# Performance work log

Hardware: AMD Instinct MI355X
Metric: run time of the kernel (lower is better)

## Reference

```python
import jax, jax.numpy as jnp
import numpy as np

B, T, TC, C, CC, H = 2, 2048, 512, 1024, 512, 16
D = C // H  # head dim = 64


def setup_inputs() -> dict:
    key = jax.random.key(0)
    ks = jax.random.split(key, 18)
    w = lambda k, i, o: (jax.random.normal(k, (i, o), jnp.float32) / np.sqrt(i).astype(np.float32))
    return {
        "x": jax.random.normal(ks[0], (B, T, C), jnp.float32),
        "cross_input": jax.random.normal(ks[1], (B, TC, CC), jnp.float32),
        "Wk": w(ks[2], C, C),  "bk": jnp.zeros((C,), jnp.float32),
        "Wq": w(ks[3], C, C),  "bq": jnp.zeros((C,), jnp.float32),
        "Wv": w(ks[4], C, C),  "bv": jnp.zeros((C,), jnp.float32),
        "Wck": w(ks[5], CC, C), "bck": jnp.zeros((C,), jnp.float32),
        "Wcq": w(ks[6], C, C),  "bcq": jnp.zeros((C,), jnp.float32),
        "Wcv": w(ks[7], CC, C), "bcv": jnp.zeros((C,), jnp.float32),
        "Wp": w(ks[8], C, C),   "bp": jnp.zeros((C,), jnp.float32),
    }


def _heads(t):
    # [B, L, C] -> [B, H, L, D]
    b, l, _ = t.shape
    return t.reshape(b, l, H, D).transpose(0, 2, 1, 3)


def reference(x, cross_input, Wk, bk, Wq, bq, Wv, bv, Wck, bck, Wcq, bcq, Wcv, bcv, Wp, bp):
    scale = np.float32(1.0 / np.sqrt(D))
    q = _heads(x @ Wq + bq)
    k = _heads(x @ Wk + bk)
    v = _heads(x @ Wv + bv)
    # causal self-attention with materialized scores (faithful to original)
    att = jnp.einsum("bhqd,bhkd->bhqk", q, k) * scale
    causal = jnp.tril(jnp.ones((T, T), bool))
    att = jnp.where(causal[None, None], att, -jnp.inf)
    y = jnp.einsum("bhqk,bhkd->bhqd", jax.nn.softmax(att, axis=-1), v)
    # cross-attention (no mask)
    qc = _heads(x @ Wcq + bcq)
    kc = _heads(cross_input @ Wck + bck)
    vc = _heads(cross_input @ Wcv + bcv)
    attc = jnp.einsum("bhqd,bhkd->bhqk", qc, kc) * scale
    y = y + jnp.einsum("bhqk,bhkd->bhqd", jax.nn.softmax(attc, axis=-1), vc)
    # merge heads + output projection (dropout prob = 0 -> identity)
    y = y.transpose(0, 2, 1, 3).reshape(x.shape[0], T, C)
    return y @ Wp + bp
```

## Files before the change

### kernel.cpp

```cpp
#include <hip/hip_runtime.h>
#include <hip/hip_bf16.h>
#include <type_traits>

typedef __bf16 bf16;
typedef __bf16 bf16x8 __attribute__((ext_vector_type(8)));
typedef float floatx4 __attribute__((ext_vector_type(4)));
typedef unsigned int uint32x4 __attribute__((ext_vector_type(4)));

#if __has_builtin(__builtin_amdgcn_exp2f)
#define EXP2(x) __builtin_amdgcn_exp2f(x)
#else
#define EXP2(x) exp2f(x)
#endif

__device__ __forceinline__ void glds16(const bf16* g, bf16* l) {
  __builtin_amdgcn_global_load_lds((const __attribute__((address_space(1))) void*)g,
                                   (__attribute__((address_space(3))) void*)l, 16, 0, 0);
}

__device__ __forceinline__ unsigned pack_bf16(float a, float b) {
  unsigned short ua = __builtin_bit_cast(unsigned short, (bf16)a);
  unsigned short ub = __builtin_bit_cast(unsigned short, (bf16)b);
  return (unsigned)ua | ((unsigned)ub << 16);
}

struct PrepArgs {
  const float* x; const float* xc;
  bf16* xbf; bf16* xcbf;
  const float* b4[4];
  const float* bc[2];
  float* bias4; float* biasc;
  const float* W[7];
  bf16* WT[7];
};

__global__ __launch_bounds__(256) void prep_kernel(PrepArgs a) {
  __shared__ bf16 tsh[32][33];
  const int bx = blockIdx.x, tid = threadIdx.x;
  if (bx < 4096) {
    int i = bx * 256 + tid;
    float4 f = ((const float4*)a.x)[i];
    bf16 t[4] = {(bf16)f.x, (bf16)f.y, (bf16)f.z, (bf16)f.w};
    *(uint2*)&a.xbf[(long)i * 4] = *(const uint2*)t;
  } else if (bx < 4608) {
    int i = (bx - 4096) * 256 + tid;
    float4 f = ((const float4*)a.xc)[i];
    bf16 t[4] = {(bf16)f.x, (bf16)f.y, (bf16)f.z, (bf16)f.w};
    *(uint2*)&a.xcbf[(long)i * 4] = *(const uint2*)t;
  } else if (bx < 4632) {
    int lb = bx - 4608;
    if (lb < 16) {
      int i = lb * 256 + tid;
      int sec = i >> 10;
      float v = a.b4[sec][i & 1023];
      if (sec == 0 || sec == 3) v *= 0.18033688f;
      a.bias4[i] = v;
    } else {
      int i = (lb - 16) * 256 + tid;
      a.biasc[i] = a.bc[i >> 10][i & 1023];
    }
  } else {
    int t = bx - 4632, w, R, bxw, byw;
    if (t < 5120) { w = t >> 10; R = 1024; int l = t & 1023; bxw = l & 31; byw = l >> 5; }
    else { int t2 = t - 5120; w = 5 + (t2 >> 9); R = 512; int l = t2 & 511; bxw = l & 31; byw = l >> 5; }
    const float* in = a.W[w];
    bf16* out = a.WT[w];
    const float sc = (w == 0 || w == 3) ? 0.18033688f : 1.0f;
    int tx = tid & 31, ty = tid >> 5;
    int c = bxw * 32 + tx;
#pragma unroll
    for (int i = 0; i < 4; i++) {
      int r = byw * 32 + ty + i * 8;
      tsh[ty + i * 8][tx] = (bf16)(in[(long)r * 1024 + c] * sc);
    }
    __syncthreads();
    int oc = byw * 32 + tx;
#pragma unroll
    for (int i = 0; i < 4; i++) {
      int orr = bxw * 32 + ty + i * 8;
      out[(long)orr * R + oc] = tsh[tx][ty + i * 8];
    }
  }
}

template <typename OutT>
__global__ __launch_bounds__(256, 3) void gemm128(const bf16* __restrict__ A,
                                                  const bf16* __restrict__ Bt,
                                                  const float* __restrict__ bias,
                                                  OutT* __restrict__ C,
                                                  int M, int N, int K, int ldc,
                                                  bf16* __restrict__ Vt,
                                                  int vcol0, int vcol1, int Lt, int tok_shift) {
  __shared__ alignas(16) bf16 As[128 * 32];
  __shared__ alignas(16) bf16 Bs[128 * 32];
  const int tid = threadIdx.x, wave = tid >> 6, lane = tid & 63;
  const int l16 = lane & 15, l4 = lane >> 4;
  const int wm = wave & 1, wn = wave >> 1;
  const int n0 = blockIdx.x * 128, m0 = blockIdx.y * 128;
  const int lrow = lane >> 2, lch = (lane & 3) * 8;

  floatx4 acc[4][4];
#pragma unroll
  for (int mt = 0; mt < 4; mt++)
#pragma unroll
    for (int nt = 0; nt < 4; nt++) acc[mt][nt] = (floatx4){0.f, 0.f, 0.f, 0.f};

  const bf16* Ag = A + (long)(m0 + wave * 32 + lrow) * K + lch;
  const bf16* Bg = Bt + (long)(n0 + wave * 32 + lrow) * K + lch;
  bf16* Al = &As[(wave * 32) * 32];
  bf16* Bl = &Bs[(wave * 32) * 32];

  for (int k0 = 0; k0 < K; k0 += 32) {
    __syncthreads();
    glds16(Ag + k0, Al);
    glds16(Ag + k0 + (long)16 * K, Al + 16 * 32);
    glds16(Bg + k0, Bl);
    glds16(Bg + k0 + (long)16 * K, Bl + 16 * 32);
    __syncthreads();
    bf16x8 a[4], b[4];
#pragma unroll
    for (int mt = 0; mt < 4; mt++) a[mt] = *(const bf16x8*)&As[(wm * 64 + mt * 16 + l16) * 32 + l4 * 8];
#pragma unroll
    for (int nt = 0; nt < 4; nt++) b[nt] = *(const bf16x8*)&Bs[(wn * 64 + nt * 16 + l16) * 32 + l4 * 8];
#pragma unroll
    for (int mt = 0; mt < 4; mt++)
#pragma unroll
      for (int nt = 0; nt < 4; nt++)
        acc[mt][nt] = __builtin_amdgcn_mfma_f32_16x16x32_bf16(a[mt], b[nt], acc[mt][nt], 0, 0, 0);
  }

  const bool vpath = (vcol0 >= 0) && (n0 >= vcol0) && (n0 < vcol1);
  if (!vpath) {
    const int coladj = (vcol0 >= 0 && n0 >= vcol1) ? (vcol1 - vcol0) : 0;
#pragma unroll
    for (int nt = 0; nt < 4; nt++) {
      int col = n0 + wn * 64 + nt * 16 + l16;
      float bv = bias[col];
#pragma unroll
      for (int mt = 0; mt < 4; mt++)
#pragma unroll
        for (int r = 0; r < 4; r++) {
          int row = m0 + wm * 64 + mt * 16 + l4 * 4 + r;
          float v = acc[mt][nt][r] + bv;
          if constexpr (std::is_same_v<OutT, float>) C[(long)row * ldc + col - coladj] = v;
          else                                       C[(long)row * ldc + col - coladj] = (bf16)v;
        }
    }
  } else {
#pragma unroll
    for (int nt = 0; nt < 4; nt++) {
      int col = n0 + wn * 64 + nt * 16 + l16;
      int c = col - vcol0, hh = c >> 6, dd = c & 63;
      float bv = bias[col];
#pragma unroll
      for (int mt = 0; mt < 4; mt++) {
        int t0 = m0 + wm * 64 + mt * 16 + l4 * 4;
        int bb = t0 >> tok_shift, t = t0 & ((1 << tok_shift) - 1);
        t = (t & ~31) | (((t >> 2) & 3) << 3) | (((t >> 4) & 1) << 2) | (t & 3);
        bf16 tmp[4];
#pragma unroll
        for (int r = 0; r < 4; r++) tmp[r] = (bf16)(acc[mt][nt][r] + bv);
        *(uint2*)&Vt[(((long)bb * 16 + hh) * 64 + dd) * Lt + t] = *(const uint2*)tmp;
      }
    }
  }
}

__global__ __launch_bounds__(256, 2) void attn_kernel(const bf16* __restrict__ QKQc,
                                                      const bf16* __restrict__ VtB,
                                                      const bf16* __restrict__ KcB,
                                                      const bf16* __restrict__ VctB,
                                                      bf16* __restrict__ Y) {
  __shared__ float2 Mbuf[4][4][16];
  __shared__ alignas(16) bf16 U[4 * 64 * 72];
  const int tid = threadIdx.x, w = tid >> 6, lane = tid & 63;
  const int l16 = lane & 15, l4 = lane >> 4;
  const int bh = blockIdx.x, h = bh & 15, b = bh >> 4;
  const int qt = 31 - (int)blockIdx.y;
  const int q0 = qt * 64;
  const int wk = w * 32;
  const float NEG = -1e30f;

  float o_self[16];

  for (int phase = 0; phase < 2; phase++) {
    const bf16 *Qb, *Kb, *Vtb;
    int kstr, vtstr, nkt;
    if (phase == 0) {
      Qb = QKQc + (long)b * 2048 * 3072 + h * 64;
      Kb = Qb + 1024;                              kstr = 3072;
      Vtb = VtB + ((long)b * 16 + h) * 64 * 2048;  vtstr = 2048;
      nkt = (qt + 2) >> 1;
    } else {
      Qb = QKQc + (long)b * 2048 * 3072 + h * 64 + 2048;
      Kb = KcB + (long)b * 512 * 1024 + h * 64;    kstr = 1024;
      Vtb = VctB + ((long)b * 16 + h) * 64 * 512;  vtstr = 512;
      nkt = 4;
    }

    __syncthreads();

    bf16x8 qf[4][2];
#pragma unroll
    for (int qtt = 0; qtt < 4; qtt++) {
      const bf16* qp = Qb + (long)(q0 + qtt * 16 + l16) * 3072 + l4 * 8;
#pragma unroll
      for (int ds = 0; ds < 2; ds++) qf[qtt][ds] = *(const bf16x8*)(qp + ds * 32);
    }

    float m_i[4], l_i[4];
#pragma unroll
    for (int qtt = 0; qtt < 4; qtt++) { m_i[qtt] = NEG; l_i[qtt] = 0.f; }
    floatx4 oacc[4][4];
#pragma unroll
    for (int mtd = 0; mtd < 4; mtd++)
#pragma unroll
      for (int qtt = 0; qtt < 4; qtt++) oacc[mtd][qtt] = (floatx4){0.f, 0.f, 0.f, 0.f};

    bf16x8 kc[2][2], kn[2][2];
#pragma unroll
    for (int mt = 0; mt < 2; mt++)
#pragma unroll
      for (int ds = 0; ds < 2; ds++)
        kc[mt][ds] = *(const bf16x8*)(Kb + (long)(wk + mt * 16 + l16) * kstr + ds * 32 + l4 * 8);

    for (int kt = 0; kt < nkt; kt++) {
      const int kbase = kt * 128 + wk;
      bf16x8 vc[4];
#pragma unroll
      for (int mtd = 0; mtd < 4; mtd++)
        vc[mtd] = *(const bf16x8*)(Vtb + (long)(mtd * 16 + l16) * vtstr + kbase + l4 * 8);

      floatx4 sacc[2][4];
#pragma unroll
      for (int mt = 0; mt < 2; mt++)
#pragma unroll
        for (int qtt = 0; qtt < 4; qtt++) sacc[mt][qtt] = (floatx4){0.f, 0.f, 0.f, 0.f};
#pragma unroll
      for (int ds = 0; ds < 2; ds++)
#pragma unroll
        for (int mt = 0; mt < 2; mt++)
#pragma unroll
          for (int qtt = 0; qtt < 4; qtt++)
            sacc[mt][qtt] = __builtin_amdgcn_mfma_f32_16x16x32_bf16(kc[mt][ds], qf[qtt][ds], sacc[mt][qtt], 0, 0, 0);

      if (kt + 1 < nkt) {
        const int nb = kbase + 128;
#pragma unroll
        for (int mt = 0; mt < 2; mt++)
#pragma unroll
          for (int ds = 0; ds < 2; ds++)
            kn[mt][ds] = *(const bf16x8*)(Kb + (long)(nb + mt * 16 + l16) * kstr + ds * 32 + l4 * 8);
      }

      if (phase == 0 && kt == nkt - 1) {
#pragma unroll
        for (int mt = 0; mt < 2; mt++) {
          int keyb = kbase + mt * 16 + l4 * 4;
#pragma unroll
          for (int qtt = 0; qtt < 4; qtt++) {
            int q = q0 + qtt * 16 + l16;
#pragma unroll
            for (int r = 0; r < 4; r++)
              if (keyb + r > q) sacc[mt][qtt][r] = NEG;
          }
        }
      }

#pragma unroll
      for (int qtt = 0; qtt < 4; qtt++) {
        float mx = fmaxf(fmaxf(fmaxf(sacc[0][qtt][0], sacc[0][qtt][1]), fmaxf(sacc[0][qtt][2], sacc[0][qtt][3])),
                         fmaxf(fmaxf(sacc[1][qtt][0], sacc[1][qtt][1]), fmaxf(sacc[1][qtt][2], sacc[1][qtt][3])));
        mx = fmaxf(mx, __shfl_xor(mx, 16));
        mx = fmaxf(mx, __shfl_xor(mx, 32));
        float mold = m_i[qtt];
        float nm = fmaxf(mx, mold);
        bool upd = nm > mold + 8.f;
        float al = upd ? EXP2(mold - nm) : 1.f;
        float mcur = upd ? nm : mold;
        m_i[qtt] = mcur;
        float p0 = EXP2(sacc[0][qtt][0] - mcur), p1 = EXP2(sacc[0][qtt][1] - mcur);
        float p2 = EXP2(sacc[0][qtt][2] - mcur), p3 = EXP2(sacc[0][qtt][3] - mcur);
        float p4 = EXP2(sacc[1][qtt][0] - mcur), p5 = EXP2(sacc[1][qtt][1] - mcur);
        float p6 = EXP2(sacc[1][qtt][2] - mcur), p7 = EXP2(sacc[1][qtt][3] - mcur);
        float rs = ((p0 + p1) + (p2 + p3)) + ((p4 + p5) + (p6 + p7));
        rs += __shfl_xor(rs, 16);
        rs += __shfl_xor(rs, 32);
        l_i[qtt] = l_i[qtt] * al + rs;
        if (__any((int)upd)) {
#pragma unroll
          for (int mtd = 0; mtd < 4; mtd++)
#pragma unroll
            for (int r = 0; r < 4; r++) oacc[mtd][qtt][r] *= al;
        }
        uint32x4 pu = {pack_bf16(p0, p1), pack_bf16(p2, p3), pack_bf16(p4, p5), pack_bf16(p6, p7)};
        bf16x8 pf = __builtin_bit_cast(bf16x8, pu);
#pragma unroll
        for (int mtd = 0; mtd < 4; mtd++)
          oacc[mtd][qtt] = __builtin_amdgcn_mfma_f32_16x16x32_bf16(vc[mtd], pf, oacc[mtd][qtt], 0, 0, 0);
      }

#pragma unroll
      for (int mt = 0; mt < 2; mt++)
#pragma unroll
        for (int ds = 0; ds < 2; ds++) kc[mt][ds] = kn[mt][ds];
    }

    if (l4 == 0) {
#pragma unroll
      for (int qtt = 0; qtt < 4; qtt++) Mbuf[w][qtt][l16] = make_float2(m_i[qtt], l_i[qtt]);
    }
    __syncthreads();
    float myscale[4], denom[4];
#pragma unroll
    for (int qtt = 0; qtt < 4; qtt++) {
      float2 s0 = Mbuf[0][qtt][l16], s1 = Mbuf[1][qtt][l16];
      float2 s2 = Mbuf[2][qtt][l16], s3 = Mbuf[3][qtt][l16];
      float M = fmaxf(fmaxf(s0.x, s1.x), fmaxf(s2.x, s3.x));
      denom[qtt] = EXP2(s0.x - M) * s0.y + EXP2(s1.x - M) * s1.y +
                   EXP2(s2.x - M) * s2.y + EXP2(s3.x - M) * s3.y;
      myscale[qtt] = EXP2(m_i[qtt] - M);
    }
#pragma unroll
    for (int qtt = 0; qtt < 4; qtt++)
#pragma unroll
      for (int mtd = 0; mtd < 4; mtd++) {
        float s = myscale[qtt];
        uint2 u = {pack_bf16(oacc[mtd][qtt][0] * s, oacc[mtd][qtt][1] * s),
                   pack_bf16(oacc[mtd][qtt][2] * s, oacc[mtd][qtt][3] * s)};
        *(uint2*)&U[((w * 64) + qtt * 16 + l16) * 72 + mtd * 16 + l4 * 4] = u;
      }
    __syncthreads();
    float sum[16];
#pragma unroll
    for (int j = 0; j < 16; j++) sum[j] = 0.f;
#pragma unroll
    for (int s = 0; s < 4; s++) {
      bf16x8 c0 = *(const bf16x8*)&U[((s * 64) + w * 16 + l16) * 72 + l4 * 16];
      bf16x8 c1 = *(const bf16x8*)&U[((s * 64) + w * 16 + l16) * 72 + l4 * 16 + 8];
#pragma unroll
      for (int j = 0; j < 8; j++) { sum[j] += (float)c0[j]; sum[8 + j] += (float)c1[j]; }
    }
    float invd = 1.0f / denom[w];
    if (phase == 0) {
#pragma unroll
      for (int j = 0; j < 16; j++) o_self[j] = sum[j] * invd;
    } else {
      long row = (long)b * 2048 + q0 + w * 16 + l16;
      bf16 out[16];
#pragma unroll
      for (int j = 0; j < 16; j++) out[j] = (bf16)(o_self[j] + sum[j] * invd);
      *(bf16x8*)&Y[row * 1024 + h * 64 + l4 * 16] = *(const bf16x8*)&out[0];
      *(bf16x8*)&Y[row * 1024 + h * 64 + l4 * 16 + 8] = *(const bf16x8*)&out[8];
    }
  }
}

extern "C" void kernel_launch(void* const* d_in, const int* in_sizes, int n_in,
                              void* d_out, int out_size, void* d_ws, size_t ws_size,
                              hipStream_t stream) {
  const float* x   = (const float*)d_in[0];
  const float* xc  = (const float*)d_in[1];
  const float* Wk  = (const float*)d_in[2];  const float* bk  = (const float*)d_in[3];
  const float* Wq  = (const float*)d_in[4];  const float* bq  = (const float*)d_in[5];
  const float* Wv  = (const float*)d_in[6];  const float* bv  = (const float*)d_in[7];
  const float* Wck = (const float*)d_in[8];  const float* bck = (const float*)d_in[9];
  const float* Wcq = (const float*)d_in[10]; const float* bcq = (const float*)d_in[11];
  const float* Wcv = (const float*)d_in[12]; const float* bcv = (const float*)d_in[13];
  const float* Wp  = (const float*)d_in[14]; const float* bp  = (const float*)d_in[15];

  char* ws = (char*)d_ws;
  const size_t MB = 1ull << 20;
  bf16*  WT_all = (bf16*)(ws + 0);
  bf16*  WC_all = (bf16*)(ws + 8 * MB);
  bf16*  WpT    = (bf16*)(ws + 10 * MB);
  bf16*  xbf    = (bf16*)(ws + 12 * MB);
  bf16*  Yb     = xbf;
  bf16*  xcbf   = (bf16*)(ws + 20 * MB);
  float* bias4  = (float*)(ws + 21 * MB);
  float* biasc  = (float*)(ws + 21 * MB + 65536);
  bf16*  QKQc   = (bf16*)(ws + 22 * MB);
  bf16*  VtB    = (bf16*)(ws + 46 * MB);
  bf16*  KcB    = (bf16*)(ws + 54 * MB);
  bf16*  VctB   = (bf16*)(ws + 56 * MB);

  PrepArgs pa;
  pa.x = x; pa.xc = xc; pa.xbf = xbf; pa.xcbf = xcbf;
  pa.b4[0] = bq; pa.b4[1] = bk; pa.b4[2] = bv; pa.b4[3] = bcq;
  pa.bc[0] = bck; pa.bc[1] = bcv;
  pa.bias4 = bias4; pa.biasc = biasc;
  pa.W[0] = Wq;  pa.WT[0] = WT_all + 0ll * 1024 * 1024;
  pa.W[1] = Wk;  pa.WT[1] = WT_all + 1ll * 1024 * 1024;
  pa.W[2] = Wv;  pa.WT[2] = WT_all + 2ll * 1024 * 1024;
  pa.W[3] = Wcq; pa.WT[3] = WT_all + 3ll * 1024 * 1024;
  pa.W[4] = Wp;  pa.WT[4] = WpT;
  pa.W[5] = Wck; pa.WT[5] = WC_all + 0ll * 1024 * 512;
  pa.W[6] = Wcv; pa.WT[6] = WC_all + 1ll * 1024 * 512;
  prep_kernel<<<10776, 256, 0, stream>>>(pa);

  gemm128<bf16><<<dim3(32, 32), 256, 0, stream>>>(xbf, WT_all, bias4, QKQc,
                                                  4096, 4096, 1024, 3072,
                                                  VtB, 2048, 3072, 2048, 11);
  gemm128<bf16><<<dim3(16, 8), 256, 0, stream>>>(xcbf, WC_all, biasc, KcB,
                                                 1024, 2048, 512, 1024,
                                                 VctB, 1024, 2048, 512, 9);

  attn_kernel<<<dim3(32, 32), 256, 0, stream>>>(QKQc, VtB, KcB, VctB, Yb);

  gemm128<float><<<dim3(8, 32), 256, 0, stream>>>(Yb, WpT, bp, (float*)d_out,
                                                  4096, 1024, 1024, 1024,
                                                  nullptr, -1, -1, 0, 0);
}
```

Measured before the change: 261.7 us.

## Software-pipeline QK^T of next tile with PV MFMAs in attention loop

Restructures the attention inner loop so the QK^T score MFMAs for the next key tile are issued after the softmax of the current tile, alongside the PV MFMAs. The first tile's scores are computed before the loop. This lets the matrix cores overlap with the exp/softmax VALU work, and the double-buffered K registers are reduced to one set. It also raises wave priority around the MFMA burst with s_setprio. The cost is more live registers (sacc and pf held across phases), which could lower occupancy.

```diff
diff --git a/kernel.cpp b/kernel.cpp
--- a/kernel.cpp
+++ b/kernel.cpp
@@ -217,40 +217,42 @@
 #pragma unroll
       for (int qtt = 0; qtt < 4; qtt++) oacc[mtd][qtt] = (floatx4){0.f, 0.f, 0.f, 0.f};
 
-    bf16x8 kc[2][2], kn[2][2];
+    bf16x8 kreg[2][2];
 #pragma unroll
     for (int mt = 0; mt < 2; mt++)
 #pragma unroll
       for (int ds = 0; ds < 2; ds++)
-        kc[mt][ds] = *(const bf16x8*)(Kb + (long)(wk + mt * 16 + l16) * kstr + ds * 32 + l4 * 8);
+        kreg[mt][ds] = *(const bf16x8*)(Kb + (long)(wk + mt * 16 + l16) * kstr + ds * 32 + l4 * 8);
+
+    floatx4 sacc[2][4];
+#pragma unroll
+    for (int mt = 0; mt < 2; mt++)
+#pragma unroll
+      for (int qtt = 0; qtt < 4; qtt++) sacc[mt][qtt] = (floatx4){0.f, 0.f, 0.f, 0.f};
+#pragma unroll
+    for (int ds = 0; ds < 2; ds++)
+#pragma unroll
+      for (int mt = 0; mt < 2; mt++)
+#pragma unroll
+        for (int qtt = 0; qtt < 4; qtt++)
+          sacc[mt][qtt] = __builtin_amdgcn_mfma_f32_16x16x32_bf16(kreg[mt][ds], qf[qtt][ds], sacc[mt][qtt], 0, 0, 0);
 
     for (int kt = 0; kt < nkt; kt++) {
       const int kbase = kt * 128 + wk;
+      const bool more = (kt + 1 < nkt);
+
       bf16x8 vc[4];
 #pragma unroll
       for (int mtd = 0; mtd < 4; mtd++)
         vc[mtd] = *(const bf16x8*)(Vtb + (long)(mtd * 16 + l16) * vtstr + kbase + l4 * 8);
 
-      floatx4 sacc[2][4];
-#pragma unroll
-      for (int mt = 0; mt < 2; mt++)
-#pragma unroll
-        for (int qtt = 0; qtt < 4; qtt++) sacc[mt][qtt] = (floatx4){0.f, 0.f, 0.f, 0.f};
-#pragma unroll
-      for (int ds = 0; ds < 2; ds++)
+      if (more) {
+        const int nb = kbase + 128;
 #pragma unroll
         for (int mt = 0; mt < 2; mt++)
 #pragma unroll
-          for (int qtt = 0; qtt < 4; qtt++)
-            sacc[mt][qtt] = __builtin_amdgcn_mfma_f32_16x16x32_bf16(kc[mt][ds], qf[qtt][ds], sacc[mt][qtt], 0, 0, 0);
-
-      if (kt + 1 < nkt) {
-        const int nb = kbase + 128;
-#pragma unroll
-        for (int mt = 0; mt < 2; mt++)
-#pragma unroll
           for (int ds = 0; ds < 2; ds++)
-            kn[mt][ds] = *(const bf16x8*)(Kb + (long)(nb + mt * 16 + l16) * kstr + ds * 32 + l4 * 8);
+            kreg[mt][ds] = *(const bf16x8*)(Kb + (long)(nb + mt * 16 + l16) * kstr + ds * 32 + l4 * 8);
       }
 
       if (phase == 0 && kt == nkt - 1) {
@@ -267,6 +269,7 @@
         }
       }
 
+      bf16x8 pf[4];
 #pragma unroll
       for (int qtt = 0; qtt < 4; qtt++) {
         float mx = fmaxf(fmaxf(fmaxf(sacc[0][qtt][0], sacc[0][qtt][1]), fmaxf(sacc[0][qtt][2], sacc[0][qtt][3])),
@@ -294,16 +297,29 @@
             for (int r = 0; r < 4; r++) oacc[mtd][qtt][r] *= al;
         }
         uint32x4 pu = {pack_bf16(p0, p1), pack_bf16(p2, p3), pack_bf16(p4, p5), pack_bf16(p6, p7)};
-        bf16x8 pf = __builtin_bit_cast(bf16x8, pu);
+        pf[qtt] = __builtin_bit_cast(bf16x8, pu);
+      }
+
+      __builtin_amdgcn_s_setprio(1);
+      if (more) {
+#pragma unroll
+        for (int mt = 0; mt < 2; mt++)
+#pragma unroll
+          for (int qtt = 0; qtt < 4; qtt++) sacc[mt][qtt] = (floatx4){0.f, 0.f, 0.f, 0.f};
+#pragma unroll
+        for (int ds = 0; ds < 2; ds++)
+#pragma unroll
+          for (int mt = 0; mt < 2; mt++)
+#pragma unroll
+            for (int qtt = 0; qtt < 4; qtt++)
+              sacc[mt][qtt] = __builtin_amdgcn_mfma_f32_16x16x32_bf16(kreg[mt][ds], qf[qtt][ds], sacc[mt][qtt], 0, 0, 0);
+      }
+#pragma unroll
+      for (int qtt = 0; qtt < 4; qtt++)
 #pragma unroll
         for (int mtd = 0; mtd < 4; mtd++)
-          oacc[mtd][qtt] = __builtin_amdgcn_mfma_f32_16x16x32_bf16(vc[mtd], pf, oacc[mtd][qtt], 0, 0, 0);
-      }
-
-#pragma unroll
-      for (int mt = 0; mt < 2; mt++)
-#pragma unroll
-        for (int ds = 0; ds < 2; ds++) kc[mt][ds] = kn[mt][ds];
+          oacc[mtd][qtt] = __builtin_amdgcn_mfma_f32_16x16x32_bf16(vc[mtd], pf[qtt], oacc[mtd][qtt], 0, 0, 0);
+      __builtin_amdgcn_s_setprio(0);
     }
 
     if (l4 == 0) {
```

Result: slower. 276.0 us (+5.5%).
